# Kernel optimization log

Measured on AMD Instinct MI355X. Metric: run time of the kernel, lower is better.

Reference implementation:

```python
import jax, jax.numpy as jnp
import numpy as np
import math

NC = 80
TOPK = 10
EPS = 1e-9
DIS = 2.5
BIG = 1e5


def _ciou(b1, b2, eps=EPS):
    # b1: (bs,1,A,4), b2: (bs,G,1,4) -> (bs,G,A)
    b1x1, b1y1, b1x2, b1y2 = b1[..., 0], b1[..., 1], b1[..., 2], b1[..., 3]
    b2x1, b2y1, b2x2, b2y2 = b2[..., 0], b2[..., 1], b2[..., 2], b2[..., 3]
    w1, h1 = b1x2 - b1x1, b1y2 - b1y1 + eps
    w2, h2 = b2x2 - b2x1, b2y2 - b2y1 + eps
    iw = jnp.clip(jnp.minimum(b1x2, b2x2) - jnp.maximum(b1x1, b2x1), 0.0)
    ih = jnp.clip(jnp.minimum(b1y2, b2y2) - jnp.maximum(b1y1, b2y1), 0.0)
    inter = iw * ih
    union = w1 * h1 + w2 * h2 - inter + eps
    iou = inter / union
    cw = jnp.maximum(b1x2, b2x2) - jnp.minimum(b1x1, b2x1)
    ch = jnp.maximum(b1y2, b2y2) - jnp.minimum(b1y1, b2y1)
    c2 = cw * cw + ch * ch + eps
    d2 = ((b2x1 + b2x2 - b1x1 - b1x2) ** 2 + (b2y1 + b2y2 - b1y1 - b1y2) ** 2) / 4.0
    v = (4.0 / math.pi ** 2) * (jnp.arctan(w2 / h2) - jnp.arctan(w1 / h1)) ** 2
    alpha = jax.lax.stop_gradient(v / (v - iou + (1.0 + eps)))
    return iou - (d2 / c2 + v * alpha)


def _cost_matrix(pred_boxes, gt_boxes, mask_gt, pred_scores, gt_labels):
    # geometric candidate masks
    pc = (pred_boxes[..., :2] + pred_boxes[..., 2:]) / 2.0  # (bs,A,2) anchor centers
    pce = pc[:, None, :, :]                                  # (bs,1,A,2)
    in_boxes = jnp.all(pce > gt_boxes[:, :, None, :2], -1) & jnp.all(gt_boxes[:, :, None, 2:] > pce, -1)
    gcen = (gt_boxes[..., :2] + gt_boxes[..., 2:]) / 2.0
    in_centers = jnp.all(pce > (gcen - DIS)[:, :, None, :], -1) & jnp.all((gcen + DIS)[:, :, None, :] > pce, -1)
    both = in_boxes & in_centers                             # (bs,G,A)

    ciou_val = _ciou(pred_boxes[:, None, :, :], gt_boxes[:, :, None, :])  # (bs,G,A)

    # summed BCE over classes against one-hot(gt_label), without (bs,G,A,nc) intermediate:
    # sum_c bce = -sum_c log(1-p_c) - (log p_y - log(1-p_y))
    p = jnp.clip(pred_scores, 1e-7, 1.0 - 1e-7)
    logp = jnp.log(p)
    log1mp = jnp.log1p(-p)
    S = -log1mp.sum(-1)                                      # (bs,A)
    delta = -(logp - log1mp)                                 # (bs,A,nc)
    per_lab = jnp.take_along_axis(jnp.transpose(delta, (0, 2, 1)), gt_labels[:, :, None], axis=1)  # (bs,G,A)
    cls_cost = S[:, None, :] + per_lab

    cost = cls_cost + 3.0 * ciou_val + BIG * (~both).astype(cost_dtype(pred_boxes))
    return cost


def cost_dtype(x):
    return x.dtype


def reference(pred_boxes, gt_boxes, mask_gt, pred_scores, gt_labels):
    cost = _cost_matrix(pred_boxes, gt_boxes, mask_gt, pred_scores, gt_labels)  # (bs,G,A)
    bs, G, A = cost.shape
    # per-GT bottom-k (lowest cost) candidate anchors
    _, idx = jax.lax.top_k(-cost, TOPK)                      # (bs,G,TOPK)
    b_ix = jnp.arange(bs)[:, None, None]
    g_ix = jnp.arange(G)[None, :, None]
    pt_mask = jnp.zeros((bs, G, A), dtype=bool).at[b_ix, g_ix, idx].set(True)
    pt_mask = pt_mask & mask_gt[:, :, None]
    # conflict resolution: anchors claimed by >1 GT go to the min-cost GT
    overlap = pt_mask.sum(1) > 1                             # (bs,A)
    pick = jnp.argmin(jnp.where(pt_mask, cost, jnp.inf), axis=1)  # (bs,A)
    pick_oh = jnp.arange(G)[None, :, None] == pick[:, None, :]    # (bs,G,A)
    final = jnp.where(overlap[:, None, :], pick_oh, pt_mask) & mask_gt[:, :, None]
    return final, cost


def setup_inputs() -> dict:
    key = jax.random.key(0)
    k = jax.random.split(key, 7)
    bs, A, G = 32, 8400, 64
    pc = jax.random.uniform(k[0], (bs, A, 2)) * 640.0
    pwh = jax.random.uniform(k[1], (bs, A, 2)) * 96.0 + 8.0
    pred_boxes = jnp.concatenate([pc - pwh / 2, pc + pwh / 2], -1)
    gc = jax.random.uniform(k[2], (bs, G, 2)) * 640.0
    gwh = jax.random.uniform(k[3], (bs, G, 2)) * 128.0 + 16.0
    gt_boxes = jnp.concatenate([gc - gwh / 2, gc + gwh / 2], -1)
    mask_gt = jax.random.uniform(k[4], (bs, G)) < 0.8
    pred_scores = jax.random.uniform(k[5], (bs, A, NC), minval=1e-4, maxval=1.0 - 1e-4)
    gt_labels = jax.random.randint(k[6], (bs, G), 0, NC, dtype=jnp.int32)
    return {"pred_boxes": pred_boxes, "gt_boxes": gt_boxes, "mask_gt": mask_gt,
            "pred_scores": pred_scores, "gt_labels": gt_labels}
```

## Files before the change

### kernel.cpp

```cpp
#include <hip/hip_runtime.h>
#include <math.h>

#define BS   32
#define A_N  8400
#define G_N  64
#define NC_N 80
#define TK   10
#define DR   48
#define DSTR 65

static __device__ __forceinline__ float fdiv(float n, float d) {
    return n * __builtin_amdgcn_rcpf(d);
}
static __device__ __forceinline__ unsigned sortable(float f) {
    unsigned u = __float_as_uint(f);
    return (u & 0x80000000u) ? ~u : (u | 0x80000000u);
}

__global__ __launch_bounds__(128)
void k_setup(const float* __restrict__ gt_boxes,
             const int*   __restrict__ gt_labels,
             float4* __restrict__ tb_box, float4* __restrict__ tb_mid,
             float4* __restrict__ tb_ctr,
             int* __restrict__ tb_ord, int* __restrict__ tb_rowk,
             int* __restrict__ tb_lab, int* __restrict__ tb_rank)
{
    __shared__ int s_lab[G_N], s_ord[G_N], s_pres[NC_N], s_rank[NC_N];
    const int b = blockIdx.x;
    const int t = threadIdx.x;

    if (t < G_N) {
        const float4 gb = ((const float4*)gt_boxes)[b * G_N + t];
        tb_box[b * G_N + t] = gb;
        const float sx = gb.x + gb.z, sy = gb.y + gb.w;
        const float w2 = gb.z - gb.x, h2 = (gb.w - gb.y) + 1e-9f;
        tb_mid[b * G_N + t] = make_float4(sx, sy, w2 * h2, atanf(w2 / h2));
        const float cx = sx / 2.0f, cy = sy / 2.0f;
        tb_ctr[b * G_N + t] = make_float4(cx - 2.5f, cy - 2.5f, cx + 2.5f, cy + 2.5f);
        const int l = gt_labels[b * G_N + t];
        s_lab[t] = l;
        tb_lab[b * G_N + t] = l;
    }
    __syncthreads();
    if (t < G_N) {
        const int myl = s_lab[t];
        int rank = 0;
        for (int j = 0; j < G_N; ++j) {
            const int lj = s_lab[j];
            rank += (lj < myl) || (lj == myl && j < t);
        }
        s_ord[rank] = t;
    }
    if (t < NC_N) {
        int p = 0;
        for (int j = 0; j < G_N; ++j) p |= (s_lab[j] == t);
        s_pres[t] = p;
    }
    __syncthreads();
    if (t < NC_N) {
        int r = 0;
        for (int c = 0; c < t; ++c) r += s_pres[c];
        const int rr = s_pres[t] ? r : -1;
        s_rank[t] = rr;
        tb_rank[b * NC_N + t] = rr;
    }
    __syncthreads();
    if (t < G_N) {
        tb_ord[b * G_N + t]  = s_ord[t];
        tb_rowk[b * G_N + t] = s_rank[s_lab[s_ord[t]]];
    }
}

__global__ __launch_bounds__(256)
void k_cost(const float* __restrict__ pred_boxes,
            const float* __restrict__ pred_scores,
            const float4* __restrict__ tb_box, const float4* __restrict__ tb_mid,
            const float4* __restrict__ tb_ctr,
            const int* __restrict__ tb_ord, const int* __restrict__ tb_rowk,
            const int* __restrict__ tb_lab, const int* __restrict__ tb_rank,
            float* __restrict__ cost)
{
    __shared__ float4 s_box[G_N];
    __shared__ float4 s_mid[G_N];
    __shared__ float4 s_ctr[G_N];
    __shared__ float4 s_pb[64];
    __shared__ float4 s_pa[64];
    __shared__ float  s_S[64 * 4];
    __shared__ float  s_delta[DR * DSTR];
    __shared__ int    s_lab[G_N], s_ord[G_N], s_rowk[G_N];
    __shared__ int    s_rank[NC_N];

    const float EPSF = 1e-9f;
    const float LO = 1e-7f;
    const float HI = (float)(1.0 - 1e-7);
    const int t = threadIdx.x;
    const int b = blockIdx.y;

    if (t < 64) {
        s_box[t]  = tb_box[b * 64 + t];
        s_ord[t]  = tb_ord[b * 64 + t];
        s_rowk[t] = tb_rowk[b * 64 + t];
        s_lab[t]  = tb_lab[b * 64 + t];
    } else if (t < 128) {
        s_mid[t - 64] = tb_mid[b * 64 + (t - 64)];
    } else if (t < 192) {
        s_ctr[t - 128] = tb_ctr[b * 64 + (t - 128)];
    }
    if (t >= 176) s_rank[t - 176] = tb_rank[b * NC_N + (t - 176)];
    __syncthreads();

    {
        const int q  = t & 3;
        const int al = t >> 2;
        const int a  = blockIdx.x * 64 + al;
        if (a < A_N) {
            const float4* p4 =
                (const float4*)(pred_scores + ((size_t)b * A_N + a) * NC_N + q * 20);
            float4 s0 = p4[0], s1 = p4[1], s2 = p4[2], s3 = p4[3], s4 = p4[4];
            s0.x=fminf(fmaxf(s0.x,LO),HI); s0.y=fminf(fmaxf(s0.y,LO),HI);
            s0.z=fminf(fmaxf(s0.z,LO),HI); s0.w=fminf(fmaxf(s0.w,LO),HI);
            s1.x=fminf(fmaxf(s1.x,LO),HI); s1.y=fminf(fmaxf(s1.y,LO),HI);
            s1.z=fminf(fmaxf(s1.z,LO),HI); s1.w=fminf(fmaxf(s1.w,LO),HI);
            s2.x=fminf(fmaxf(s2.x,LO),HI); s2.y=fminf(fmaxf(s2.y,LO),HI);
            s2.z=fminf(fmaxf(s2.z,LO),HI); s2.w=fminf(fmaxf(s2.w,LO),HI);
            s3.x=fminf(fmaxf(s3.x,LO),HI); s3.y=fminf(fmaxf(s3.y,LO),HI);
            s3.z=fminf(fmaxf(s3.z,LO),HI); s3.w=fminf(fmaxf(s3.w,LO),HI);
            s4.x=fminf(fmaxf(s4.x,LO),HI); s4.y=fminf(fmaxf(s4.y,LO),HI);
            s4.z=fminf(fmaxf(s4.z,LO),HI); s4.w=fminf(fmaxf(s4.w,LO),HI);
            float g1 = (1.0f-s0.x); g1*=(1.0f-s0.y); g1*=(1.0f-s0.z); g1*=(1.0f-s0.w);
            g1*=(1.0f-s1.x); g1*=(1.0f-s1.y); g1*=(1.0f-s1.z); g1*=(1.0f-s1.w);
            float g2 = (1.0f-s2.x); g2*=(1.0f-s2.y); g2*=(1.0f-s2.z); g2*=(1.0f-s2.w);
            g2*=(1.0f-s3.x); g2*=(1.0f-s3.y); g2*=(1.0f-s3.z); g2*=(1.0f-s3.w);
            float g3 = (1.0f-s4.x); g3*=(1.0f-s4.y); g3*=(1.0f-s4.z); g3*=(1.0f-s4.w);
            s_S[al * 4 + q] = (__logf(g1) + __logf(g2)) + __logf(g3);
            const float pv[20] = {s0.x,s0.y,s0.z,s0.w, s1.x,s1.y,s1.z,s1.w,
                                  s2.x,s2.y,s2.z,s2.w, s3.x,s3.y,s3.z,s3.w,
                                  s4.x,s4.y,s4.z,s4.w};
            #pragma unroll
            for (int i = 0; i < 20; ++i) {
                const int r = s_rank[q * 20 + i];
                if (r >= 0 && r < DR)
                    s_delta[r * DSTR + al] =
                        __logf((1.0f - pv[i]) * __builtin_amdgcn_rcpf(pv[i]));
            }
            if (q == 0) {
                const float4 pb = ((const float4*)pred_boxes)[(size_t)b * A_N + a];
                s_pb[al] = pb;
                const float pcx = (pb.x + pb.z) / 2.0f;
                const float pcy = (pb.y + pb.w) / 2.0f;
                const float w1  = pb.z - pb.x;
                const float h1  = (pb.w - pb.y) + EPSF;
                s_pa[al] = make_float4(pcx, pcy, w1 * h1, atanf(w1 / h1));
            }
        }
    }
    __syncthreads();

    const int la = t & 63;
    const int gs = t >> 6;
    const int a  = blockIdx.x * 64 + la;
    if (a >= A_N) return;

    const float4 pb = s_pb[la];
    const float4 pa = s_pa[la];
    const float4 Sq = ((const float4*)s_S)[la];
    const float S = -(((Sq.x + Sq.y) + Sq.z) + Sq.w);
    const float KPI = (float)(4.0 / (M_PI * M_PI));
    const float* prow = pred_scores + ((size_t)b * A_N + a) * NC_N;
    float* crow = cost + (size_t)b * G_N * A_N + a;
    const float pcx = pa.x, pcy = pa.y, area1 = pa.z, atp = pa.w;

    #pragma unroll 4
    for (int k = gs * 16; k < gs * 16 + 16; ++k) {
        const int g = s_ord[k];
        const int r = s_rowk[k];
        float delta;
        if (r < DR) {
            delta = s_delta[r * DSTR + la];
        } else {
            const float pc = fminf(fmaxf(prow[s_lab[g]], LO), HI);
            delta = __logf((1.0f - pc) * __builtin_amdgcn_rcpf(pc));
        }
        const float Sd = S + delta;
        const float4 gb = s_box[g];
        const float4 gm = s_mid[g];
        const float4 gc = s_ctr[g];

        const bool inb  = (pcx > gb.x) && (pcy > gb.y) && (gb.z > pcx) && (gb.w > pcy);
        const bool inc  = (pcx > gc.x) && (pcy > gc.y) && (gc.z > pcx) && (gc.w > pcy);
        const bool both = inb && inc;

        const float iw    = fmaxf(fminf(pb.z, gb.z) - fmaxf(pb.x, gb.x), 0.0f);
        const float ih    = fmaxf(fminf(pb.w, gb.w) - fmaxf(pb.y, gb.y), 0.0f);
        const float inter = iw * ih;
        const float uni   = ((area1 + gm.z) - inter) + EPSF;
        const float iou   = fdiv(inter, uni);
        const float cw    = fmaxf(pb.z, gb.z) - fminf(pb.x, gb.x);
        const float ch    = fmaxf(pb.w, gb.w) - fminf(pb.y, gb.y);
        const float c2    = ((cw * cw) + (ch * ch)) + EPSF;
        const float dx    = (gm.x - pb.x) - pb.z;
        const float dy    = (gm.y - pb.y) - pb.w;
        const float d2    = ((dx * dx) + (dy * dy)) / 4.0f;
        const float dif   = gm.w - atp;
        const float v     = KPI * (dif * dif);
        const float alpha = fdiv(v, (v - iou) + 1.0f);
        const float ciou  = iou - (fdiv(d2, c2) + v * alpha);

        const float cst   = (Sd + 3.0f * ciou) + (both ? 0.0f : 100000.0f);
        crow[(size_t)g * A_N] = cst;
    }
}

__global__ __launch_bounds__(256)
void k_init(uint4* __restrict__ slt, long ns4)
{
    const long stride = (long)gridDim.x * 256;
    const uint4 m4 = make_uint4(~0u, ~0u, ~0u, ~0u);
    for (long i = (long)blockIdx.x * 256 + threadIdx.x; i < ns4; i += stride)
        slt[i] = m4;
}

__global__ __launch_bounds__(256)
void k_topk(const float* __restrict__ cost,
            const unsigned char* __restrict__ mask_gt,
            int* __restrict__ topk,
            unsigned long long* __restrict__ slot)
{
    __shared__ unsigned long long s_w[4][TK];

    const int bg   = blockIdx.x;
    const int t    = threadIdx.x;
    const int lane = t & 63;
    const int wid  = t >> 6;
    const float* row = cost + (size_t)bg * A_N;
    const unsigned long long UMAX = ~0ull;

    unsigned long long v[TK];
    #pragma unroll
    for (int j = 0; j < TK; ++j) v[j] = UMAX;

    auto consider = [&](float c, int idx) {
        const unsigned long long key =
            ((unsigned long long)sortable(c) << 14) | (unsigned)idx;
        if (key < v[TK - 1]) {
            v[TK - 1] = key;
            #pragma unroll
            for (int j = TK - 2; j >= 0; --j) {
                const bool sw = v[j + 1] < v[j];
                const unsigned long long tv = v[j];
                v[j]     = sw ? v[j + 1] : v[j];
                v[j + 1] = sw ? tv : v[j + 1];
            }
        }
    };

    const float4* row4 = (const float4*)row;
    const int NV = A_N / 4;
    float4 cur = make_float4(0.f, 0.f, 0.f, 0.f);
    if (t < NV) cur = row4[t];
    for (int i = t; i < NV; i += 256) {
        const int i2 = i + 256;
        float4 nxt = make_float4(0.f, 0.f, 0.f, 0.f);
        if (i2 < NV) nxt = row4[i2];
        const int base = i * 4;
        consider(cur.x, base);
        consider(cur.y, base + 1);
        consider(cur.z, base + 2);
        consider(cur.w, base + 3);
        cur = nxt;
    }

    #pragma unroll
    for (int r = 0; r < TK; ++r) {
        unsigned long long bv = v[0];
        #pragma unroll
        for (int off = 1; off < 64; off <<= 1) {
            const unsigned long long ov = __shfl_xor(bv, off, 64);
            bv = (ov < bv) ? ov : bv;
        }
        if (lane == 0) s_w[wid][r] = bv;
        if (v[0] == bv) {
            #pragma unroll
            for (int j = 0; j < TK - 1; ++j) v[j] = v[j + 1];
            v[TK - 1] = UMAX;
        }
    }
    __syncthreads();

    if (wid == 0) {
        const int b = bg >> 6, g = bg & 63;
        const int msk = (int)mask_gt[bg];
        unsigned long long cv = UMAX;
        if (lane < 4 * TK) cv = s_w[lane / TK][lane % TK];
        #pragma unroll
        for (int r = 0; r < TK; ++r) {
            unsigned long long bv = cv;
            #pragma unroll
            for (int off = 1; off < 64; off <<= 1) {
                const unsigned long long ov = __shfl_xor(bv, off, 64);
                bv = (ov < bv) ? ov : bv;
            }
            if (lane == 0) {
                const int a = (int)(bv & 16383ull);
                topk[bg * TK + r] = a;
                if (msk) {
                    const unsigned long long key = ((bv >> 14) << 6) | (unsigned)g;
                    atomicMin(&slot[(size_t)b * A_N + a], key);
                }
            }
            if (cv == bv) cv = UMAX;
        }
    }
}

__global__ __launch_bounds__(256)
void k_fin(const unsigned long long* __restrict__ slot,
           float* __restrict__ final_out)
{
    const int i = blockIdx.x * 256 + threadIdx.x;
    const int b = blockIdx.y;
    if (i >= A_N / 4) return;

    const unsigned long long* sp = slot + (size_t)b * A_N + i * 4;
    int w0 = -1, w1 = -1, w2 = -1, w3 = -1;
    {
        const unsigned long long s0 = sp[0], s1 = sp[1], s2 = sp[2], s3 = sp[3];
        if (s0 != ~0ull) w0 = (int)(s0 & 63ull);
        if (s1 != ~0ull) w1 = (int)(s1 & 63ull);
        if (s2 != ~0ull) w2 = (int)(s2 & 63ull);
        if (s3 != ~0ull) w3 = (int)(s3 & 63ull);
    }
    float4* fp = (float4*)(final_out + (size_t)b * G_N * A_N) + i;
    for (int g = 0; g < G_N; ++g) {
        const float4 o = make_float4(w0 == g ? 1.0f : 0.0f,
                                     w1 == g ? 1.0f : 0.0f,
                                     w2 == g ? 1.0f : 0.0f,
                                     w3 == g ? 1.0f : 0.0f);
        fp[(size_t)g * (A_N / 4)] = o;
    }
}

extern "C" void kernel_launch(void* const* d_in, const int* in_sizes, int n_in,
                              void* d_out, int out_size, void* d_ws, size_t ws_size,
                              hipStream_t stream)
{
    const float* pred_boxes  = (const float*)d_in[0];
    const float* gt_boxes    = (const float*)d_in[1];
    const unsigned char* mask_gt = (const unsigned char*)d_in[2];
    const float* pred_scores = (const float*)d_in[3];
    const int*   gt_labels   = (const int*)d_in[4];

    float* out_final = (float*)d_out;
    float* out_cost  = out_final + (size_t)BS * G_N * A_N;

    size_t off = 0;
    auto alloc = [&](size_t bytes) {
        void* p = (char*)d_ws + off;
        off += (bytes + 255) & ~(size_t)255;
        return p;
    };
    unsigned long long* slot = (unsigned long long*)alloc((size_t)BS * A_N * 8);
    int*    topk_ws = (int*)   alloc((size_t)BS * G_N * TK * 4);
    float4* tb_box  = (float4*)alloc((size_t)BS * G_N * 16);
    float4* tb_mid  = (float4*)alloc((size_t)BS * G_N * 16);
    float4* tb_ctr  = (float4*)alloc((size_t)BS * G_N * 16);
    int*    tb_ord  = (int*)   alloc((size_t)BS * G_N * 4);
    int*    tb_rowk = (int*)   alloc((size_t)BS * G_N * 4);
    int*    tb_lab  = (int*)   alloc((size_t)BS * G_N * 4);
    int*    tb_rank = (int*)   alloc((size_t)BS * NC_N * 4);
    (void)off;

    const long ns4 = (long)BS * A_N / 2;
    k_init <<<dim3(132), 256, 0, stream>>>((uint4*)slot, ns4);
    k_setup<<<dim3(BS), 128, 0, stream>>>(gt_boxes, gt_labels,
                                          tb_box, tb_mid, tb_ctr,
                                          tb_ord, tb_rowk, tb_lab, tb_rank);
    k_cost <<<dim3((A_N + 63) / 64, BS), 256, 0, stream>>>(
        pred_boxes, pred_scores, tb_box, tb_mid, tb_ctr,
        tb_ord, tb_rowk, tb_lab, tb_rank, out_cost);
    k_topk <<<dim3(BS * G_N), 256, 0, stream>>>(out_cost, mask_gt, topk_ws, slot);
    k_fin  <<<dim3((A_N / 4 + 255) / 256, BS), 256, 0, stream>>>(slot, out_final);
}
```

Before: 290.5 us.

## Fuse slot init into setup, presort GT tables, read uniformly from global

Folds the slot-initialisation kernel into the setup kernel, which saves one launch. Setup now writes the GT box, mid and center tables already permuted into label order, plus a packed (rank, g) pair. The cost kernel reads these through a wave-uniform (readfirstlane) index instead of staging them in LDS. The delta table is enlarged to cover all 64 possible distinct labels, which removes the global pred_scores fallback path at the cost of more LDS and more log evaluations per anchor.

```diff
diff --git a/kernel.cpp b/kernel.cpp
--- a/kernel.cpp
+++ b/kernel.cpp
@@ -6,7 +6,7 @@
 #define G_N  64
 #define NC_N 80
 #define TK   10
-#define DR   48
+#define DR   64
 #define DSTR 65
 
 static __device__ __forceinline__ float fdiv(float n, float d) {
@@ -17,30 +17,27 @@
     return (u & 0x80000000u) ? ~u : (u | 0x80000000u);
 }
 
-__global__ __launch_bounds__(128)
+__global__ __launch_bounds__(256)
 void k_setup(const float* __restrict__ gt_boxes,
              const int*   __restrict__ gt_labels,
-             float4* __restrict__ tb_box, float4* __restrict__ tb_mid,
-             float4* __restrict__ tb_ctr,
-             int* __restrict__ tb_ord, int* __restrict__ tb_rowk,
-             int* __restrict__ tb_lab, int* __restrict__ tb_rank)
+             float4* __restrict__ tb_sb, float4* __restrict__ tb_sm,
+             float4* __restrict__ tb_sc, int2* __restrict__ tb_mt,
+             int* __restrict__ tb_rank,
+             uint4* __restrict__ slt, long ns4)
 {
     __shared__ int s_lab[G_N], s_ord[G_N], s_pres[NC_N], s_rank[NC_N];
-    const int b = blockIdx.x;
+    const int blk = blockIdx.x;
     const int t = threadIdx.x;
 
-    if (t < G_N) {
-        const float4 gb = ((const float4*)gt_boxes)[b * G_N + t];
-        tb_box[b * G_N + t] = gb;
-        const float sx = gb.x + gb.z, sy = gb.y + gb.w;
-        const float w2 = gb.z - gb.x, h2 = (gb.w - gb.y) + 1e-9f;
-        tb_mid[b * G_N + t] = make_float4(sx, sy, w2 * h2, atanf(w2 / h2));
-        const float cx = sx / 2.0f, cy = sy / 2.0f;
-        tb_ctr[b * G_N + t] = make_float4(cx - 2.5f, cy - 2.5f, cx + 2.5f, cy + 2.5f);
-        const int l = gt_labels[b * G_N + t];
-        s_lab[t] = l;
-        tb_lab[b * G_N + t] = l;
-    }
+    {
+        const long stride = (long)gridDim.x * 256;
+        const uint4 m4 = make_uint4(~0u, ~0u, ~0u, ~0u);
+        for (long i = (long)blk * 256 + t; i < ns4; i += stride) slt[i] = m4;
+    }
+    if (blk >= BS) return;
+    const int b = blk;
+
+    if (t < G_N) s_lab[t] = gt_labels[b * G_N + t];
     __syncthreads();
     if (t < G_N) {
         const int myl = s_lab[t];
@@ -66,28 +63,30 @@
     }
     __syncthreads();
     if (t < G_N) {
-        tb_ord[b * G_N + t]  = s_ord[t];
-        tb_rowk[b * G_N + t] = s_rank[s_lab[s_ord[t]]];
+        const int g = s_ord[t];
+        const float4 gb = ((const float4*)gt_boxes)[b * G_N + g];
+        tb_sb[b * G_N + t] = gb;
+        const float sx = gb.x + gb.z, sy = gb.y + gb.w;
+        const float w2 = gb.z - gb.x, h2 = (gb.w - gb.y) + 1e-9f;
+        tb_sm[b * G_N + t] = make_float4(sx, sy, w2 * h2, atanf(w2 / h2));
+        const float cx = sx / 2.0f, cy = sy / 2.0f;
+        tb_sc[b * G_N + t] = make_float4(cx - 2.5f, cy - 2.5f, cx + 2.5f, cy + 2.5f);
+        tb_mt[b * G_N + t] = make_int2(s_rank[s_lab[g]], g);
     }
 }
 
 __global__ __launch_bounds__(256)
 void k_cost(const float* __restrict__ pred_boxes,
             const float* __restrict__ pred_scores,
-            const float4* __restrict__ tb_box, const float4* __restrict__ tb_mid,
-            const float4* __restrict__ tb_ctr,
-            const int* __restrict__ tb_ord, const int* __restrict__ tb_rowk,
-            const int* __restrict__ tb_lab, const int* __restrict__ tb_rank,
+            const float4* __restrict__ tb_sb, const float4* __restrict__ tb_sm,
+            const float4* __restrict__ tb_sc, const int2* __restrict__ tb_mt,
+            const int* __restrict__ tb_rank,
             float* __restrict__ cost)
 {
-    __shared__ float4 s_box[G_N];
-    __shared__ float4 s_mid[G_N];
-    __shared__ float4 s_ctr[G_N];
     __shared__ float4 s_pb[64];
     __shared__ float4 s_pa[64];
     __shared__ float  s_S[64 * 4];
     __shared__ float  s_delta[DR * DSTR];
-    __shared__ int    s_lab[G_N], s_ord[G_N], s_rowk[G_N];
     __shared__ int    s_rank[NC_N];
 
     const float EPSF = 1e-9f;
@@ -96,17 +95,7 @@
     const int t = threadIdx.x;
     const int b = blockIdx.y;
 
-    if (t < 64) {
-        s_box[t]  = tb_box[b * 64 + t];
-        s_ord[t]  = tb_ord[b * 64 + t];
-        s_rowk[t] = tb_rowk[b * 64 + t];
-        s_lab[t]  = tb_lab[b * 64 + t];
-    } else if (t < 128) {
-        s_mid[t - 64] = tb_mid[b * 64 + (t - 64)];
-    } else if (t < 192) {
-        s_ctr[t - 128] = tb_ctr[b * 64 + (t - 128)];
-    }
-    if (t >= 176) s_rank[t - 176] = tb_rank[b * NC_N + (t - 176)];
+    if (t < NC_N) s_rank[t] = tb_rank[b * NC_N + t];
     __syncthreads();
 
     {
@@ -139,7 +128,7 @@
             #pragma unroll
             for (int i = 0; i < 20; ++i) {
                 const int r = s_rank[q * 20 + i];
-                if (r >= 0 && r < DR)
+                if (r >= 0)
                     s_delta[r * DSTR + al] =
                         __logf((1.0f - pv[i]) * __builtin_amdgcn_rcpf(pv[i]));
             }
@@ -166,25 +155,23 @@
     const float4 Sq = ((const float4*)s_S)[la];
     const float S = -(((Sq.x + Sq.y) + Sq.z) + Sq.w);
     const float KPI = (float)(4.0 / (M_PI * M_PI));
-    const float* prow = pred_scores + ((size_t)b * A_N + a) * NC_N;
     float* crow = cost + (size_t)b * G_N * A_N + a;
     const float pcx = pa.x, pcy = pa.y, area1 = pa.z, atp = pa.w;
 
+    const float4* sbp = tb_sb + b * G_N;
+    const float4* smp = tb_sm + b * G_N;
+    const float4* scp = tb_sc + b * G_N;
+    const int2*   mtp = tb_mt + b * G_N;
+
     #pragma unroll 4
     for (int k = gs * 16; k < gs * 16 + 16; ++k) {
-        const int g = s_ord[k];
-        const int r = s_rowk[k];
-        float delta;
-        if (r < DR) {
-            delta = s_delta[r * DSTR + la];
-        } else {
-            const float pc = fminf(fmaxf(prow[s_lab[g]], LO), HI);
-            delta = __logf((1.0f - pc) * __builtin_amdgcn_rcpf(pc));
-        }
+        const int ku = __builtin_amdgcn_readfirstlane(k);
+        const float4 gb = sbp[ku];
+        const float4 gm = smp[ku];
+        const float4 gc = scp[ku];
+        const int2   mt = mtp[ku];
+        const float delta = s_delta[mt.x * DSTR + la];
         const float Sd = S + delta;
-        const float4 gb = s_box[g];
-        const float4 gm = s_mid[g];
-        const float4 gc = s_ctr[g];
 
         const bool inb  = (pcx > gb.x) && (pcy > gb.y) && (gb.z > pcx) && (gb.w > pcy);
         const bool inc  = (pcx > gc.x) && (pcy > gc.y) && (gc.z > pcx) && (gc.w > pcy);
@@ -207,17 +194,8 @@
         const float ciou  = iou - (fdiv(d2, c2) + v * alpha);
 
         const float cst   = (Sd + 3.0f * ciou) + (both ? 0.0f : 100000.0f);
-        crow[(size_t)g * A_N] = cst;
-    }
-}
-
-__global__ __launch_bounds__(256)
-void k_init(uint4* __restrict__ slt, long ns4)
-{
-    const long stride = (long)gridDim.x * 256;
-    const uint4 m4 = make_uint4(~0u, ~0u, ~0u, ~0u);
-    for (long i = (long)blockIdx.x * 256 + threadIdx.x; i < ns4; i += stride)
-        slt[i] = m4;
+        crow[(size_t)mt.y * A_N] = cst;
+    }
 }
 
 __global__ __launch_bounds__(256)
@@ -361,23 +339,19 @@
     };
     unsigned long long* slot = (unsigned long long*)alloc((size_t)BS * A_N * 8);
     int*    topk_ws = (int*)   alloc((size_t)BS * G_N * TK * 4);
-    float4* tb_box  = (float4*)alloc((size_t)BS * G_N * 16);
-    float4* tb_mid  = (float4*)alloc((size_t)BS * G_N * 16);
-    float4* tb_ctr  = (float4*)alloc((size_t)BS * G_N * 16);
-    int*    tb_ord  = (int*)   alloc((size_t)BS * G_N * 4);
-    int*    tb_rowk = (int*)   alloc((size_t)BS * G_N * 4);
-    int*    tb_lab  = (int*)   alloc((size_t)BS * G_N * 4);
+    float4* tb_sb   = (float4*)alloc((size_t)BS * G_N * 16);
+    float4* tb_sm   = (float4*)alloc((size_t)BS * G_N * 16);
+    float4* tb_sc   = (float4*)alloc((size_t)BS * G_N * 16);
+    int2*   tb_mt   = (int2*)  alloc((size_t)BS * G_N * 8);
     int*    tb_rank = (int*)   alloc((size_t)BS * NC_N * 4);
     (void)off;
 
     const long ns4 = (long)BS * A_N / 2;
-    k_init <<<dim3(132), 256, 0, stream>>>((uint4*)slot, ns4);
-    k_setup<<<dim3(BS), 128, 0, stream>>>(gt_boxes, gt_labels,
-                                          tb_box, tb_mid, tb_ctr,
-                                          tb_ord, tb_rowk, tb_lab, tb_rank);
+    k_setup<<<dim3(132), 256, 0, stream>>>(gt_boxes, gt_labels,
+                                           tb_sb, tb_sm, tb_sc, tb_mt, tb_rank,
+                                           (uint4*)slot, ns4);
     k_cost <<<dim3((A_N + 63) / 64, BS), 256, 0, stream>>>(
-        pred_boxes, pred_scores, tb_box, tb_mid, tb_ctr,
-        tb_ord, tb_rowk, tb_lab, tb_rank, out_cost);
+        pred_boxes, pred_scores, tb_sb, tb_sm, tb_sc, tb_mt, tb_rank, out_cost);
     k_topk <<<dim3(BS * G_N), 256, 0, stream>>>(out_cost, mask_gt, topk_ws, slot);
     k_fin  <<<dim3((A_N / 4 + 255) / 256, BS), 256, 0, stream>>>(slot, out_final);
 }
```

Result: no change. 292.1 us (+0.5%).
